# Performance work log

Hardware: AMD Instinct MI355X
Metric: run time of the kernel (lower is better)

Reference implementation:

```python
import jax, jax.numpy as jnp
import numpy as np

N1, E1 = 50000, 400000   # drug graph nodes/edges
N2, E2 = 50000, 400000   # second-branch nodes/edges
G = 256                   # number of graphs in the batch
F1, F2 = 93, 43           # node feature dims


def setup_inputs() -> dict:
    key = jax.random.key(0)
    ks = jax.random.split(key, 40)
    rn = lambda k, s, sc=0.05: jax.random.normal(k, s, dtype=jnp.float32) * sc
    inp = {}
    inp["data"] = 0  # unused placeholder arg in the original forward
    inp["x"] = jax.random.normal(ks[0], (N1, F1), dtype=jnp.float32)
    inp["edge_index"] = jax.random.randint(ks[1], (2, E1), 0, N1)
    inp["batch"] = jnp.sort(jax.random.randint(ks[2], (N1,), 0, G))
    inp["a"] = jax.random.normal(ks[3], (N2, F2), dtype=jnp.float32)
    inp["edge"] = jax.random.randint(ks[4], (2, E2), 0, N2)
    inp["c"] = jnp.sort(jax.random.randint(ks[5], (N2,), 0, G))
    # GINConv linear weights (x @ W + b convention)
    inp["W1"] = rn(ks[6], (F1, F1));        inp["b1"] = rn(ks[7], (F1,))
    inp["W2"] = rn(ks[8], (F1, F1 * 10));   inp["b2"] = rn(ks[9], (F1 * 10,))
    inp["W3"] = rn(ks[10], (F2, F2));       inp["b3"] = rn(ks[11], (F2,))
    inp["W4"] = rn(ks[12], (F2, F2 * 10));  inp["b4"] = rn(ks[13], (F2 * 10,))
    # fc_g: 1860 -> 1024 -> 512 ; fc_g1: 860 -> 1024 -> 512
    inp["fcg_w1"] = rn(ks[14], (F1 * 10 * 2, 1024)); inp["fcg_b1"] = rn(ks[15], (1024,))
    inp["fcg_w2"] = rn(ks[16], (1024, 512));         inp["fcg_b2"] = rn(ks[17], (512,))
    inp["fcg1_w1"] = rn(ks[18], (F2 * 10 * 2, 1024)); inp["fcg1_b1"] = rn(ks[19], (1024,))
    inp["fcg1_w2"] = rn(ks[20], (1024, 512));         inp["fcg1_b2"] = rn(ks[21], (512,))
    # fc_final / fc_final1: 512 -> 256 -> 1
    inp["ff_w1"] = rn(ks[22], (512, 256)); inp["ff_b1"] = rn(ks[23], (256,))
    inp["ff_w2"] = rn(ks[24], (256, 1));   inp["ff_b2"] = rn(ks[25], (1,))
    inp["ff1_w1"] = rn(ks[26], (512, 256)); inp["ff1_b1"] = rn(ks[27], (256,))
    inp["ff1_w2"] = rn(ks[28], (256, 1));   inp["ff1_b2"] = rn(ks[29], (1,))
    return inp


def _gin(h, ei, W, b):
    # PyG GINConv(eps=0): Linear(x_i + sum_{j->i} x_j)
    agg = jax.ops.segment_sum(h[ei[0]], ei[1], num_segments=h.shape[0])
    return (h + agg) @ W + b


def _pool(h, seg):
    # concat(global_max_pool, global_mean_pool) per graph -> [G, 2*d]
    s = jax.ops.segment_sum(h, seg, num_segments=G)
    cnt = jax.ops.segment_sum(jnp.ones((h.shape[0], 1), h.dtype), seg, num_segments=G)
    mean = s / jnp.maximum(cnt, 1.0)
    mx = jax.ops.segment_max(h, seg, num_segments=G)
    mx = jnp.where(jnp.isfinite(mx), mx, 0.0)
    return jnp.concatenate([mx, mean], axis=1)


def reference(data, x, edge_index, batch, a, edge, c,
              W1, b1, W2, b2, W3, b3, W4, b4,
              fcg_w1, fcg_b1, fcg_w2, fcg_b2,
              fcg1_w1, fcg1_b1, fcg1_w2, fcg1_b2,
              ff_w1, ff_b1, ff_w2, ff_b2,
              ff1_w1, ff1_b1, ff1_w2, ff1_b2):
    relu = jax.nn.relu
    # branch 1 (93-dim features)
    h = relu(_gin(x, edge_index, W1, b1))
    h = relu(_gin(h, edge_index, W2, b2))          # [N1, 930]
    p = _pool(h, batch)                             # [G, 1860]
    x_g = relu(p @ fcg_w1 + fcg_b1) @ fcg_w2 + fcg_b2   # [G, 512] (dropout = identity at eval)
    z = relu(x_g @ ff_w1 + ff_b1) @ ff_w2 + ff_b2        # [G, 1]
    # branch 2 (43-dim features)
    h1 = relu(_gin(a, edge, W3, b3))
    h1 = relu(_gin(h1, edge, W4, b4))               # [N2, 430]
    p1 = _pool(h1, c)                                # [G, 860]
    x_g1 = relu(p1 @ fcg1_w1 + fcg1_b1) @ fcg1_w2 + fcg1_b2  # [G, 512]
    z1 = relu(x_g1 @ ff1_w1 + ff1_b1) @ ff1_w2 + ff1_b2       # [G, 1]
    return (z, x_g, x_g1, z1)
```

## Files before the change

kernel.cpp:

```cpp
#include <hip/hip_runtime.h>


static constexpr int NG  = 256;
static constexpr int CHK = 4096;

typedef short  short8  __attribute__((ext_vector_type(8)));
typedef float  floatx4 __attribute__((ext_vector_type(4)));

__device__ __forceinline__ short f2bf(float f) {
    unsigned u = __float_as_uint(f);
    u += 0x7fff + ((u >> 16) & 1);
    return (short)(u >> 16);
}
__device__ __forceinline__ float bf2f(unsigned short s) {
    return __uint_as_float((unsigned)s << 16);
}
__device__ __forceinline__ float bf_lo(unsigned u) { return __uint_as_float(u << 16); }
__device__ __forceinline__ float bf_hi(unsigned u) { return __uint_as_float(u & 0xffff0000u); }

static inline int cdiv(int a, int b) { return (a + b - 1) / b; }

__global__ void offs_both_kernel(const int* __restrict__ s1, int n1, int* __restrict__ o1,
                                 const int* __restrict__ s2, int n2, int* __restrict__ o2) {
    int t = blockIdx.x * 256 + threadIdx.x;
    int br = t >> 9;
    int g = t & 511;
    if (br > 1 || g > NG) return;
    const int* seg = br ? s2 : s1;
    int N = br ? n2 : n1;
    int* offs = br ? o2 : o1;
    int lo = 0, hi = N;
    while (lo < hi) {
        int mid = (lo + hi) >> 1;
        if (seg[mid] < g) lo = mid + 1; else hi = mid;
    }
    offs[g] = lo;
}

__device__ __forceinline__ void deg_win_dev(const int* __restrict__ ei, int E, int N,
                                            int* __restrict__ deg, int bid) {
    int win = bid & 7, chunk = bid >> 3;
    int e0 = chunk * CHK;
    int e1 = e0 + CHK; if (e1 > E) e1 = E;
    int wlo = (int)((long)win * N / 8);
    int whi = (int)((long)(win + 1) * N / 8);
    for (int e = e0 + threadIdx.x; e < e1; e += 256) {
        int dst = ei[E + e];
        if (dst >= wlo && dst < whi) atomicAdd(&deg[dst], 1);
    }
}

__global__ __launch_bounds__(256) void deg_win_both_kernel(
        const int* ei1, int E1, int N1, int* d1, int nblk1,
        const int* ei2, int E2, int N2, int* d2) {
    int bid = blockIdx.x;
    if (bid < nblk1) deg_win_dev(ei1, E1, N1, d1, bid);
    else             deg_win_dev(ei2, E2, N2, d2, bid - nblk1);
}

__global__ __launch_bounds__(256) void scan1_both_kernel(
        const int* __restrict__ d1, int N1, int* __restrict__ x1, int* __restrict__ bs1, int nb1,
        const int* __restrict__ d2, int N2, int* __restrict__ x2, int* __restrict__ bs2) {
    __shared__ int sh[256];
    const int* deg; int* excl; int* bsum; int N; int blk;
    if ((int)blockIdx.x < nb1) { deg = d1; excl = x1; bsum = bs1; N = N1; blk = blockIdx.x; }
    else { deg = d2; excl = x2; bsum = bs2; N = N2; blk = blockIdx.x - nb1; }
    int base = blk * 1024;
    int t = threadIdx.x;
    int v[4];
    int s = 0;
    #pragma unroll
    for (int i = 0; i < 4; ++i) {
        int idx = base + t * 4 + i;
        v[i] = s;
        s += (idx < N) ? deg[idx] : 0;
    }
    sh[t] = s;
    __syncthreads();
    for (int off = 1; off < 256; off <<= 1) {
        int xv = (t >= off) ? sh[t - off] : 0;
        __syncthreads();
        sh[t] += xv;
        __syncthreads();
    }
    int texcl = (t > 0) ? sh[t - 1] : 0;
    #pragma unroll
    for (int i = 0; i < 4; ++i) {
        int idx = base + t * 4 + i;
        if (idx < N) excl[idx] = texcl + v[i];
    }
    if (t == 255) bsum[blk] = sh[255];
}

__global__ void scan2_both_kernel(int* __restrict__ b1, int nb1,
                                  int* __restrict__ b2, int nb2) {
    if (threadIdx.x) return;
    int* b = blockIdx.x ? b2 : b1;
    int nb = blockIdx.x ? nb2 : nb1;
    int acc = 0;
    for (int i = 0; i < nb; ++i) { int t = b[i]; b[i] = acc; acc += t; }
}

__global__ void scan3_both_kernel(int* __restrict__ x1, const int* __restrict__ bs1,
                                  int* __restrict__ c1, int N1, int Ev1,
                                  int* __restrict__ x2, const int* __restrict__ bs2,
                                  int* __restrict__ c2, int N2, int Ev2, int nc1) {
    int bid = blockIdx.x;
    int* excl; const int* bsum; int* cur; int N, E, i;
    if (bid < nc1) { i = bid * 256 + threadIdx.x; excl = x1; bsum = bs1; cur = c1; N = N1; E = Ev1; }
    else { i = (bid - nc1) * 256 + threadIdx.x; excl = x2; bsum = bs2; cur = c2; N = N2; E = Ev2; }
    if (i < N) {
        int v = excl[i] + bsum[i >> 10];
        excl[i] = v;
        cur[i] = v;
    }
    if (i == 0) excl[N] = E;
}

__device__ __forceinline__ void fill_win_dev(const int* __restrict__ ei, int E, int N,
                                             int* __restrict__ cursor, int* __restrict__ csr,
                                             int bid) {
    int win = bid & 7, chunk = bid >> 3;
    int e0 = chunk * CHK;
    int e1 = e0 + CHK; if (e1 > E) e1 = E;
    int wlo = (int)((long)win * N / 8);
    int whi = (int)((long)(win + 1) * N / 8);
    for (int e = e0 + threadIdx.x; e < e1; e += 256) {
        int dst = ei[E + e];
        if (dst >= wlo && dst < whi) {
            int pos = atomicAdd(&cursor[dst], 1);
            csr[pos] = ei[e];
        }
    }
}

__global__ __launch_bounds__(256) void fill_win_both_kernel(
        const int* ei1, int E1, int N1, int* c1, int* s1, int nblk1,
        const int* ei2, int E2, int N2, int* c2, int* s2) {
    int bid = blockIdx.x;
    if (bid < nblk1) fill_win_dev(ei1, E1, N1, c1, s1, bid);
    else             fill_win_dev(ei2, E2, N2, c2, s2, bid - nblk1);
}

struct RJob { const float* W; short* Wb; int K, Nsrc, Ndst, KP; };
struct RJobs10 { RJob j[10]; };

__global__ __launch_bounds__(256) void repack_all_kernel(RJobs10 jobs) {
    __shared__ __align__(16) short sh[64][72];
    RJob jb = jobs.j[blockIdx.y];
    int tilesC = (jb.Ndst + 63) >> 6;
    int tilesK = (jb.KP + 63) >> 6;
    if ((int)blockIdx.x >= tilesC * tilesK) return;
    int c0 = ((int)blockIdx.x % tilesC) * 64;
    int k0 = ((int)blockIdx.x / tilesC) * 64;
    int t = threadIdx.x;
    #pragma unroll 4
    for (int idx = t; idx < 64 * 64; idx += 256) {
        int kk = idx >> 6, cc = idx & 63;
        int k = k0 + kk, cg = c0 + cc;
        float v = (k < jb.K && cg < jb.Nsrc) ? jb.W[(size_t)k * jb.Nsrc + cg] : 0.f;
        sh[cc][kk] = f2bf(v);
    }
    __syncthreads();
    int kt = jb.KP - k0; if (kt > 64) kt = 64;
    int chunks = kt >> 3;
    for (int idx = t; idx < 64 * chunks; idx += 256) {
        int cc = idx / chunks, ch = idx - cc * chunks;
        int cg = c0 + cc;
        if (cg < jb.Ndst) {
            uint4 v = *(const uint4*)&sh[cc][ch * 8];
            *(uint4*)&jb.Wb[(size_t)cg * jb.KP + k0 + ch * 8] = v;
        }
    }
}

__global__ __launch_bounds__(256) void cast_both_kernel(
        const float* __restrict__ x1, unsigned short* __restrict__ xb1, int N1,
        const float* __restrict__ x2, unsigned short* __restrict__ xb2, int N2) {
    int idx = blockIdx.x * 256 + threadIdx.x;
    int tot1 = N1 * 96;
    if (idx < tot1) {
        int n = idx / 96, k = idx - n * 96;
        float v = (k < 93) ? x1[(size_t)n * 93 + k] : 0.f;
        xb1[idx] = (unsigned short)f2bf(v);
    } else {
        idx -= tot1;
        if (idx < N2 * 48) {
            int n = idx / 48, k = idx - n * 48;
            float v = (k < 43) ? x2[(size_t)n * 43 + k] : 0.f;
            xb2[idx] = (unsigned short)f2bf(v);
        }
    }
}

template<int F, int FP, int FA, int GROUPS>
__device__ __forceinline__ void gather_dev(
        const unsigned short* __restrict__ xb, const int* __restrict__ csr,
        const int* __restrict__ ro, float* __restrict__ agg, int N, int bid) {
    int wave = (bid * 256 + threadIdx.x) >> 6;
    int lane = threadIdx.x & 63;
    if (wave >= N) return;
    constexpr int HW = FP / 2;
    const unsigned* base = (const unsigned*)xb;
    int s = ro[wave], e = ro[wave + 1];
    int grp, l;
    if (GROUPS == 2) { grp = lane >> 5; l = lane & 31; }
    else             { grp = 0;         l = lane;      }
    bool act = l < HW;
    float lo = 0.f, hi = 0.f;
    int i = s + grp;
    if (GROUPS == 1) {
        for (; i + 3 < e; i += 4) {
            int n0 = csr[i], n1 = csr[i + 1], n2 = csr[i + 2], n3 = csr[i + 3];
            unsigned u0 = act ? base[(size_t)n0 * HW + l] : 0u;
            unsigned u1 = act ? base[(size_t)n1 * HW + l] : 0u;
            unsigned u2 = act ? base[(size_t)n2 * HW + l] : 0u;
            unsigned u3 = act ? base[(size_t)n3 * HW + l] : 0u;
            lo += bf_lo(u0) + bf_lo(u1) + bf_lo(u2) + bf_lo(u3);
            hi += bf_hi(u0) + bf_hi(u1) + bf_hi(u2) + bf_hi(u3);
        }
        for (; i < e; ++i) {
            int n0 = csr[i];
            unsigned u0 = act ? base[(size_t)n0 * HW + l] : 0u;
            lo += bf_lo(u0); hi += bf_hi(u0);
        }
    } else {
        for (; i + 2 < e; i += 4) {
            int n0 = csr[i], n1 = csr[i + 2];
            unsigned u0 = act ? base[(size_t)n0 * HW + l] : 0u;
            unsigned u1 = act ? base[(size_t)n1 * HW + l] : 0u;
            lo += bf_lo(u0) + bf_lo(u1);
            hi += bf_hi(u0) + bf_hi(u1);
        }
        if (i < e) {
            int n0 = csr[i];
            unsigned u0 = act ? base[(size_t)n0 * HW + l] : 0u;
            lo += bf_lo(u0); hi += bf_hi(u0);
        }
        lo += __shfl_xor(lo, 32, 64);
        hi += __shfl_xor(hi, 32, 64);
    }
    if (grp == 0) {
        int cidx = 2 * l;
        if (cidx + 1 < F)
            *(float2*)&agg[(size_t)wave * FA + cidx] = make_float2(lo, hi);
        else if (cidx < F)
            agg[(size_t)wave * FA + cidx] = lo;
    }
}

__global__ __launch_bounds__(256) void gather_both_kernel(
        const unsigned short* xb1, const int* csr1, const int* ro1, float* agg1, int N1, int nblk1,
        const unsigned short* xb2, const int* csr2, const int* ro2, float* agg2, int N2) {
    int bid = blockIdx.x;
    if (bid < nblk1) gather_dev<93, 96, 94, 1>(xb1, csr1, ro1, agg1, N1, bid);
    else             gather_dev<43, 48, 44, 2>(xb2, csr2, ro2, agg2, N2, bid - nblk1);
}

template<int F, int KP, int NT, int FP, int FA>
__device__ __forceinline__ void gin_linear_dev(
        const float* __restrict__ x, const float* __restrict__ agg,
        const short* __restrict__ Wb, const float* __restrict__ b,
        unsigned short* __restrict__ h1b, int N, int blk, short* Vb) {
    constexpr int KK = KP / 32;
    int c0 = blk * 64;
    int tid = threadIdx.x;
    int wid = tid >> 6;
    int lane = tid & 63;
    int ln = lane & 15, quad = lane >> 4;
    int cvalid = N - c0; if (cvalid > 64) cvalid = 64;
    for (int i = tid; i < 64 * (KP - F); i += 256)
        Vb[(i / (KP - F)) * KP + F + i % (KP - F)] = 0;
    int nelem = cvalid * F;
    const float* xs = x + (size_t)c0 * F;
    const float* as = agg + (size_t)c0 * FA;
    for (int idx = tid; idx < nelem; idx += 256) {
        int r = idx / F, k = idx - r * F;
        Vb[r * KP + k] = f2bf(xs[idx] + as[r * FA + k]);
    }
    __syncthreads();
    short8 afr[KK][4];
    #pragma unroll
    for (int kk = 0; kk < KK; ++kk)
        #pragma unroll
        for (int ms = 0; ms < 4; ++ms)
            afr[kk][ms] = *(const short8*)&Vb[(ms * 16 + ln) * KP + kk * 32 + quad * 8];
    for (int nt = wid; nt < NT; nt += 4) {
        int col = nt * 16 + ln;
        float bcol = (col < F) ? b[col] : 0.f;
        short8 bfr[KK];
        const short8* bp = (const short8*)(Wb + (size_t)col * KP + quad * 8);
        #pragma unroll
        for (int kk = 0; kk < KK; ++kk) bfr[kk] = bp[kk * 4];
        #pragma unroll
        for (int ms = 0; ms < 4; ++ms) {
            if (ms * 16 < cvalid) {
                floatx4 acc = {0.f, 0.f, 0.f, 0.f};
                #pragma unroll
                for (int kk = 0; kk < KK; ++kk)
                    acc = __builtin_amdgcn_mfma_f32_16x16x32_bf16(
                              afr[kk][ms], bfr[kk], acc, 0, 0, 0);
                #pragma unroll
                for (int r = 0; r < 4; ++r) {
                    int row = ms * 16 + quad * 4 + r;
                    if (row < cvalid) {
                        unsigned short hv = 0;
                        if (col < F) hv = (unsigned short)f2bf(fmaxf(acc[r] + bcol, 0.f));
                        h1b[(size_t)(c0 + row) * FP + col] = hv;
                    }
                }
            }
        }
    }
}

__global__ __launch_bounds__(256) void gin_linear_both_kernel(
        const float* x1, const float* agg1, const short* Wbl1, const float* bb1,
        unsigned short* h1b1, int N1, int nblk1,
        const float* x2, const float* agg2, const short* Wbl2, const float* bb2,
        unsigned short* h1b2, int N2) {
    __shared__ __align__(16) short Vb[64 * 96];
    int bid = blockIdx.x;
    if (bid < nblk1)
        gin_linear_dev<93, 96, 6, 96, 94>(x1, agg1, Wbl1, bb1, h1b1, N1, bid, Vb);
    else
        gin_linear_dev<43, 64, 3, 48, 44>(x2, agg2, Wbl2, bb2, h1b2, N2, bid - nblk1, Vb);
}

template<int F, int KP, int FO, int NT, int NS, int FP, int FA>
__device__ __forceinline__ void gin_pool_dev(
        const unsigned short* __restrict__ h1b, const float* __restrict__ agg,
        const short* __restrict__ Wb, const float* __restrict__ b,
        const int* __restrict__ offs,
        float* __restrict__ ppmax, float* __restrict__ ppsum,
        int blk, short* Vb, float* pmaxL, float* psumL) {
    constexpr int KK = KP / 32;
    int g = blk / NS;
    int s = blk % NS;
    int tid = threadIdx.x;
    int wid = tid >> 6;
    int lane = tid & 63;
    int ln = lane & 15;
    int quad = lane >> 4;

    int gs0 = offs[g], ge0 = offs[g + 1];
    int per = (ge0 - gs0 + NS - 1) / NS;
    int gs = gs0 + s * per;
    int ge = gs + per; if (ge > ge0) ge = ge0;

    for (int i = tid; i < NT * 16; i += 256) { pmaxL[i] = 0.f; psumL[i] = 0.f; }
    for (int i = tid; i < 64 * (KP - F); i += 256)
        Vb[(i / (KP - F)) * KP + F + i % (KP - F)] = 0;

    for (int c0 = gs; c0 < ge; c0 += 64) {
        __syncthreads();
        int cvalid = ge - c0; if (cvalid > 64) cvalid = 64;
        int nelem = cvalid * F;
        const unsigned short* hs = h1b + (size_t)c0 * FP;
        const float* as = agg + (size_t)c0 * FA;
        for (int idx = tid; idx < nelem; idx += 256) {
            int r = idx / F, k = idx - r * F;
            Vb[r * KP + k] = f2bf(bf2f(hs[r * FP + k]) + as[r * FA + k]);
        }
        __syncthreads();
        short8 afr[KK][4];
        #pragma unroll
        for (int kk = 0; kk < KK; ++kk)
            #pragma unroll
            for (int ms = 0; ms < 4; ++ms)
                afr[kk][ms] = *(const short8*)&Vb[(ms * 16 + ln) * KP + kk * 32 + quad * 8];
        for (int nt = wid; nt < NT; nt += 4) {
            int col = nt * 16 + ln;
            float bcol = (col < FO) ? b[col] : 0.f;
            short8 bfr[KK];
            const short8* bp = (const short8*)(Wb + (size_t)col * KP + quad * 8);
            #pragma unroll
            for (int kk = 0; kk < KK; ++kk) bfr[kk] = bp[kk * 4];
            float cmx = 0.f, csm = 0.f;
            #pragma unroll
            for (int ms = 0; ms < 4; ++ms) {
                if (ms * 16 < cvalid) {
                    floatx4 acc = {0.f, 0.f, 0.f, 0.f};
                    #pragma unroll
                    for (int kk = 0; kk < KK; ++kk)
                        acc = __builtin_amdgcn_mfma_f32_16x16x32_bf16(
                                  afr[kk][ms], bfr[kk], acc, 0, 0, 0);
                    #pragma unroll
                    for (int r = 0; r < 4; ++r) {
                        int rowl = ms * 16 + quad * 4 + r;
                        float v = fmaxf(acc[r] + bcol, 0.f);
                        if (rowl < cvalid) { cmx = fmaxf(cmx, v); csm += v; }
                    }
                }
            }
            cmx = fmaxf(cmx, __shfl_xor(cmx, 16, 64));
            cmx = fmaxf(cmx, __shfl_xor(cmx, 32, 64));
            csm += __shfl_xor(csm, 16, 64);
            csm += __shfl_xor(csm, 32, 64);
            if (quad == 0) {
                int i = nt * 16 + ln;
                pmaxL[i] = fmaxf(pmaxL[i], cmx);
                psumL[i] += csm;
            }
        }
    }
    __syncthreads();
    float* om = ppmax + (size_t)(g * NS + s) * FO;
    float* os = ppsum + (size_t)(g * NS + s) * FO;
    for (int col = tid; col < FO; col += 256) { om[col] = pmaxL[col]; os[col] = psumL[col]; }
}

__global__ __launch_bounds__(256) void gin_pool_both_kernel(
        const unsigned short* h1b1, const float* agg1, const short* Wbg1, const float* b21,
        const int* offs1, float* pm1, float* ps1, int nblk1,
        const unsigned short* h1b2, const float* agg2, const short* Wbg2, const float* b22,
        const int* offs2, float* pm2, float* ps2) {
    __shared__ __align__(16) short Vb[64 * 96];
    __shared__ float pmaxL[944];
    __shared__ float psumL[944];
    int bid = blockIdx.x;
    if (bid < nblk1)
        gin_pool_dev<93, 96, 930, 59, 4, 96, 94>(h1b1, agg1, Wbg1, b21, offs1,
                                                 pm1, ps1, bid, Vb, pmaxL, psumL);
    else
        gin_pool_dev<43, 64, 430, 27, 4, 48, 44>(h1b2, agg2, Wbg2, b22, offs2,
                                                 pm2, ps2, bid - nblk1, Vb, pmaxL, psumL);
}

template<int FO, int NS, int KPAD>
__device__ __forceinline__ void pool_reduce_dev(
        const float* __restrict__ ppmax, const float* __restrict__ ppsum,
        const int* __restrict__ offs, short* __restrict__ pb, int g) {
    int cntg = offs[g + 1] - offs[g];
    float den = (float)(cntg > 0 ? cntg : 1);
    for (int col = threadIdx.x; col < KPAD; col += 256) {
        float v = 0.f;
        if (col < FO) {
            float m = 0.f;
            #pragma unroll
            for (int ss = 0; ss < NS; ++ss)
                m = fmaxf(m, ppmax[(size_t)(g * NS + ss) * FO + col]);
            v = m;
        } else if (col < 2 * FO) {
            float sm = 0.f;
            #pragma unroll
            for (int ss = 0; ss < NS; ++ss)
                sm += ppsum[(size_t)(g * NS + ss) * FO + (col - FO)];
            v = sm / den;
        }
        pb[(size_t)g * KPAD + col] = f2bf(v);
    }
}

__global__ __launch_bounds__(256) void pool_reduce_both_kernel(
        const float* pm1, const float* ps1, const int* offs1, short* pb1,
        const float* pm2, const float* ps2, const int* offs2, short* pb2) {
    int bid = blockIdx.x;
    if (bid < NG) pool_reduce_dev<930, 4, 2048>(pm1, ps1, offs1, pb1, bid);
    else          pool_reduce_dev<430, 4, 1024>(pm2, ps2, offs2, pb2, bid - NG);
}

template<int KPC>
__device__ __forceinline__ void fc_mfma_dev(
        const short* __restrict__ Ab, const short* __restrict__ Wb,
        float* __restrict__ partial, int KP, int NB, int bid) {
    int mb = bid & 3;
    int nb = (bid >> 2) % NB;
    int ks = (bid >> 2) / NB;
    int tid = threadIdx.x;
    int w = tid >> 6;
    int lane = tid & 63;
    int ln = lane & 15, quad = lane >> 4;
    int row = mb * 64 + w * 16 + ln;
    const short* ap = Ab + (size_t)row * KP + ks * KPC + quad * 8;
    const short* wp = Wb + (size_t)(nb * 64 + ln) * KP + ks * KPC + quad * 8;
    floatx4 acc[4];
    #pragma unroll
    for (int ns = 0; ns < 4; ++ns) acc[ns] = {0.f, 0.f, 0.f, 0.f};
    #pragma unroll
    for (int kk = 0; kk < KPC / 32; ++kk) {
        short8 a = *(const short8*)(ap + kk * 32);
        #pragma unroll
        for (int ns = 0; ns < 4; ++ns) {
            short8 b = *(const short8*)(wp + (size_t)ns * 16 * KP + kk * 32);
            acc[ns] = __builtin_amdgcn_mfma_f32_16x16x32_bf16(a, b, acc[ns], 0, 0, 0);
        }
    }
    int N = NB * 64;
    float* pp = partial + ((size_t)ks * 256 + mb * 64 + w * 16) * N + nb * 64;
    #pragma unroll
    for (int ns = 0; ns < 4; ++ns)
        #pragma unroll
        for (int r = 0; r < 4; ++r)
            pp[(quad * 4 + r) * N + ns * 16 + ln] = acc[ns][r];
}

template<int KPC1, int KPC2>
__global__ __launch_bounds__(256) void fc_mfma_both_kernel(
        const short* A1, const short* B1, float* P1, int KPa, int NBa, int nblk1,
        const short* A2, const short* B2, float* P2, int KPb, int NBb) {
    int bid = blockIdx.x;
    if (bid < nblk1) fc_mfma_dev<KPC1>(A1, B1, P1, KPa, NBa, bid);
    else             fc_mfma_dev<KPC2>(A2, B2, P2, KPb, NBb, bid - nblk1);
}

template<int KS, bool RELU, bool WBF16, bool WF32>
__global__ __launch_bounds__(256) void fc_reduce_both_kernel(
        const float* __restrict__ P1, const float* __restrict__ b1v,
        short* __restrict__ ob1, float* __restrict__ of1, int MN1, int Nn1,
        const float* __restrict__ P2, const float* __restrict__ b2v,
        short* __restrict__ ob2, float* __restrict__ of2, int MN2, int Nn2) {
    int idx = blockIdx.x * 256 + threadIdx.x;
    const float* P; const float* bias; short* ob; float* of; int MN, Nn;
    if (idx < MN1) { P = P1; bias = b1v; ob = ob1; of = of1; MN = MN1; Nn = Nn1; }
    else {
        idx -= MN1;
        if (idx >= MN2) return;
        P = P2; bias = b2v; ob = ob2; of = of2; MN = MN2; Nn = Nn2;
    }
    float v = bias[idx % Nn];
    #pragma unroll
    for (int s = 0; s < KS; ++s) v += P[(size_t)s * MN + idx];
    if (RELU) v = fmaxf(v, 0.f);
    if (WBF16) ob[idx] = f2bf(v);
    if (WF32)  of[idx] = v;
}

template<int KS>
__global__ __launch_bounds__(256) void head_final_both_kernel(
        const float* __restrict__ P1, const float* __restrict__ b11,
        const float* __restrict__ w21, const float* __restrict__ b21,
        float* __restrict__ z1o,
        const float* __restrict__ P2, const float* __restrict__ b12,
        const float* __restrict__ w22, const float* __restrict__ b22,
        float* __restrict__ z2o) {
    int br = blockIdx.x >> 8;
    int row = blockIdx.x & 255;
    const float* P  = br ? P2  : P1;
    const float* b1 = br ? b12 : b11;
    const float* w2 = br ? w22 : w21;
    const float* b2 = br ? b22 : b21;
    float* zo       = br ? z2o : z1o;
    int t = threadIdx.x;
    float v = b1[t];
    int idx = row * 256 + t;
    #pragma unroll
    for (int s = 0; s < KS; ++s) v += P[(size_t)s * 65536 + idx];
    v = fmaxf(v, 0.f) * w2[t];
    #pragma unroll
    for (int o = 32; o > 0; o >>= 1) v += __shfl_down(v, o, 64);
    __shared__ float red[4];
    if ((t & 63) == 0) red[t >> 6] = v;
    __syncthreads();
    if (t == 0) zo[row] = red[0] + red[1] + red[2] + red[3] + b2[0];
}

extern "C" void kernel_launch(void* const* d_in, const int* in_sizes, int n_in,
                              void* d_out, int out_size, void* d_ws, size_t ws_size,
                              hipStream_t stream) {
    (void)n_in; (void)out_size; (void)ws_size;
    const float* x      = (const float*)d_in[1];
    const int*   ei     = (const int*)  d_in[2];
    const int*   batch  = (const int*)  d_in[3];
    const float* a      = (const float*)d_in[4];
    const int*   ed     = (const int*)  d_in[5];
    const int*   c      = (const int*)  d_in[6];
    const float* W1  = (const float*)d_in[7],  *b1  = (const float*)d_in[8];
    const float* W2  = (const float*)d_in[9],  *b2  = (const float*)d_in[10];
    const float* W3  = (const float*)d_in[11], *b3  = (const float*)d_in[12];
    const float* W4  = (const float*)d_in[13], *b4  = (const float*)d_in[14];
    const float* fg_w1  = (const float*)d_in[15], *fg_b1  = (const float*)d_in[16];
    const float* fg_w2  = (const float*)d_in[17], *fg_b2  = (const float*)d_in[18];
    const float* fg1_w1 = (const float*)d_in[19], *fg1_b1 = (const float*)d_in[20];
    const float* fg1_w2 = (const float*)d_in[21], *fg1_b2 = (const float*)d_in[22];
    const float* ff_w1  = (const float*)d_in[23], *ff_b1  = (const float*)d_in[24];
    const float* ff_w2  = (const float*)d_in[25], *ff_b2  = (const float*)d_in[26];
    const float* ff1_w1 = (const float*)d_in[27], *ff1_b1 = (const float*)d_in[28];
    const float* ff1_w2 = (const float*)d_in[29], *ff1_b2 = (const float*)d_in[30];

    const int N1 = in_sizes[1] / 93;
    const int E1 = in_sizes[2] / 2;
    const int N2 = in_sizes[4] / 43;
    const int E2 = in_sizes[5] / 2;

    float* out = (float*)d_out;
    float* z   = out;
    float* xg  = out + 256;
    float* xg1 = out + 256 + 256 * 512;
    float* z1  = out + 256 + 2 * 256 * 512;

    char* wsb = (char*)d_ws;
    size_t off = 0;
    auto carve = [&](size_t bytes) {
        void* ptr = wsb + off;
        off = (off + bytes + 255) & ~(size_t)255;
        return ptr;
    };
    float*          agg1 = (float*)carve((size_t)N1 * 94 * sizeof(float));
    float*          agg2 = (float*)carve((size_t)N2 * 44 * sizeof(float));
    unsigned short* xb1  = (unsigned short*)carve((size_t)N1 * 96 * 2);
    unsigned short* xb2  = (unsigned short*)carve((size_t)N2 * 48 * 2);
    unsigned short* h1b1 = (unsigned short*)carve((size_t)N1 * 96 * 2);
    unsigned short* h1b2 = (unsigned short*)carve((size_t)N2 * 48 * 2);
    short* pb1  = (short*)carve((size_t)NG * 2048 * 2);
    short* pb2  = (short*)carve((size_t)NG * 1024 * 2);
    short* t1b1 = (short*)carve((size_t)NG * 1024 * 2);
    short* t1b2 = (short*)carve((size_t)NG * 1024 * 2);
    short* xgb1 = (short*)carve((size_t)NG * 512 * 2);
    short* xgb2 = (short*)carve((size_t)NG * 512 * 2);
    short* Wbl1 = (short*)carve((size_t)96 * 96 * 2);
    short* Wbg1 = (short*)carve((size_t)944 * 96 * 2);
    short* Wbl2 = (short*)carve((size_t)48 * 64 * 2);
    short* Wbg2 = (short*)carve((size_t)432 * 64 * 2);
    short* Wb1a = (short*)carve((size_t)1024 * 2048 * 2);
    short* Wb2a = (short*)carve((size_t)512 * 1024 * 2);
    short* Wb3a = (short*)carve((size_t)256 * 512 * 2);
    short* Wb1b = (short*)carve((size_t)1024 * 1024 * 2);
    short* Wb2b = (short*)carve((size_t)512 * 1024 * 2);
    short* Wb3b = (short*)carve((size_t)256 * 512 * 2);
    int* offs1 = (int*)carve(257 * 4);
    int* offs2 = (int*)carve(257 * 4);
    int* deg   = (int*)carve((size_t)(N1 + N2) * 4);
    int* rowoff1 = (int*)carve((size_t)(N1 + 1) * 4);
    int* rowoff2 = (int*)carve((size_t)(N2 + 1) * 4);
    int* cursor1 = (int*)carve((size_t)N1 * 4);
    int* cursor2 = (int*)carve((size_t)N2 * 4);
    int* csr1  = (int*)carve((size_t)E1 * 4);
    int* csr2  = (int*)carve((size_t)E2 * 4);
    int* bsum  = (int*)carve(256 * 4);
    int* deg1 = deg, *deg2 = deg + N1;
    int* bsum1 = bsum, *bsum2 = bsum + 128;
    float* partial1 = agg1;
    float* partial2 = agg1 + (size_t)8 * 262144;
    float* pm1 = (float*)xb1;
    float* ps1 = pm1 + (size_t)NG * 4 * 930;
    float* pm2 = (float*)xb2;
    float* ps2 = pm2 + (size_t)NG * 4 * 430;

    constexpr int KS = 8;

    RJobs10 jobs = {{
        { W1,     Wbl1, 93,   93,   96,   96   },
        { W2,     Wbg1, 93,   930,  944,  96   },
        { W3,     Wbl2, 43,   43,   48,   64   },
        { W4,     Wbg2, 43,   430,  432,  64   },
        { fg_w1,  Wb1a, 1860, 1024, 1024, 2048 },
        { fg_w2,  Wb2a, 1024, 512,  512,  1024 },
        { ff_w1,  Wb3a, 512,  256,  256,  512  },
        { fg1_w1, Wb1b, 860,  1024, 1024, 1024 },
        { fg1_w2, Wb2b, 1024, 512,  512,  1024 },
        { ff1_w1, Wb3b, 512,  256,  256,  512  },
    }};
    repack_all_kernel<<<dim3(512, 10), 256, 0, stream>>>(jobs);
    cast_both_kernel<<<cdiv(N1 * 96 + N2 * 48, 256), 256, 0, stream>>>(
        x, xb1, N1, a, xb2, N2);
    offs_both_kernel<<<4, 256, 0, stream>>>(batch, N1, offs1, c, N2, offs2);
    hipMemsetAsync(deg, 0, (size_t)(N1 + N2) * 4, stream);
    int nwb1 = cdiv(E1, CHK) * 8, nwb2 = cdiv(E2, CHK) * 8;
    deg_win_both_kernel<<<nwb1 + nwb2, 256, 0, stream>>>(ei, E1, N1, deg1, nwb1,
                                                         ed, E2, N2, deg2);
    int nb1 = cdiv(N1, 1024), nb2 = cdiv(N2, 1024);
    scan1_both_kernel<<<nb1 + nb2, 256, 0, stream>>>(deg1, N1, rowoff1, bsum1, nb1,
                                                     deg2, N2, rowoff2, bsum2);
    scan2_both_kernel<<<2, 64, 0, stream>>>(bsum1, nb1, bsum2, nb2);
    int nc1 = cdiv(N1, 256), nc2 = cdiv(N2, 256);
    scan3_both_kernel<<<nc1 + nc2, 256, 0, stream>>>(rowoff1, bsum1, cursor1, N1, E1,
                                                     rowoff2, bsum2, cursor2, N2, E2, nc1);
    fill_win_both_kernel<<<nwb1 + nwb2, 256, 0, stream>>>(ei, E1, N1, cursor1, csr1, nwb1,
                                                          ed, E2, N2, cursor2, csr2);

    int ng1 = cdiv(N1, 4), ng2 = cdiv(N2, 4);
    gather_both_kernel<<<ng1 + ng2, 256, 0, stream>>>(
        xb1, csr1, rowoff1, agg1, N1, ng1, xb2, csr2, rowoff2, agg2, N2);
    int nl1 = cdiv(N1, 64), nl2 = cdiv(N2, 64);
    gin_linear_both_kernel<<<nl1 + nl2, 256, 0, stream>>>(
        x, agg1, Wbl1, b1, h1b1, N1, nl1, a, agg2, Wbl2, b3, h1b2, N2);
    gather_both_kernel<<<ng1 + ng2, 256, 0, stream>>>(
        h1b1, csr1, rowoff1, agg1, N1, ng1, h1b2, csr2, rowoff2, agg2, N2);
    gin_pool_both_kernel<<<NG * 4 * 2, 256, 0, stream>>>(
        h1b1, agg1, Wbg1, b2, offs1, pm1, ps1, NG * 4,
        h1b2, agg2, Wbg2, b4, offs2, pm2, ps2);
    pool_reduce_both_kernel<<<2 * NG, 256, 0, stream>>>(
        pm1, ps1, offs1, pb1, pm2, ps2, offs2, pb2);

    fc_mfma_both_kernel<256, 128><<<1024, 256, 0, stream>>>(
        pb1, Wb1a, partial1, 2048, 16, 512, pb2, Wb1b, partial2, 1024, 16);
    fc_reduce_both_kernel<KS, true, true, false><<<cdiv(2 * 256 * 1024, 256), 256, 0, stream>>>(
        partial1, fg_b1, t1b1, nullptr, 256 * 1024, 1024,
        partial2, fg1_b1, t1b2, nullptr, 256 * 1024, 1024);
    fc_mfma_both_kernel<128, 128><<<512, 256, 0, stream>>>(
        t1b1, Wb2a, partial1, 1024, 8, 256, t1b2, Wb2b, partial2, 1024, 8);
    fc_reduce_both_kernel<KS, false, true, true><<<cdiv(2 * 256 * 512, 256), 256, 0, stream>>>(
        partial1, fg_b2, xgb1, xg, 256 * 512, 512,
        partial2, fg1_b2, xgb2, xg1, 256 * 512, 512);
    fc_mfma_both_kernel<64, 64><<<256, 256, 0, stream>>>(
        xgb1, Wb3a, partial1, 512, 4, 128, xgb2, Wb3b, partial2, 512, 4);
    head_final_both_kernel<KS><<<512, 256, 0, stream>>>(
        partial1, ff_b1, ff_w2, ff_b2, z,
        partial2, ff1_b1, ff1_w2, ff1_b2, z1);
}
```

Baseline: 451.2 us.

## Fuse self-term into gather and emit bf16 GIN inputs directly

The gather kernel now adds each node's own feature row to the neighbour sum and writes the combined (x + agg) row as padded bf16, instead of writing a float aggregate. The linear and pool kernels then load MFMA A-fragments straight from global bf16 rows, dropping the LDS staging, the float-to-bf16 combine loop and a barrier per tile. This cuts intermediate traffic (fp32 agg to bf16) and deepens gather unrolling to 8 loads in flight. The combined sum is rounded to bf16 once, which was also true of the old path. Split-K partial buffers get their own allocation, since agg no longer exists to alias.

```diff
diff --git a/kernel.cpp b/kernel.cpp
--- a/kernel.cpp
+++ b/kernel.cpp
@@ -11,9 +11,6 @@
     unsigned u = __float_as_uint(f);
     u += 0x7fff + ((u >> 16) & 1);
     return (short)(u >> 16);
-}
-__device__ __forceinline__ float bf2f(unsigned short s) {
-    return __uint_as_float((unsigned)s << 16);
 }
 __device__ __forceinline__ float bf_lo(unsigned u) { return __uint_as_float(u << 16); }
 __device__ __forceinline__ float bf_hi(unsigned u) { return __uint_as_float(u & 0xffff0000u); }
@@ -193,75 +190,93 @@
     }
 }
 
-template<int F, int FP, int FA, int GROUPS>
+template<int FP, int GROUPS>
 __device__ __forceinline__ void gather_dev(
-        const unsigned short* __restrict__ xb, const int* __restrict__ csr,
-        const int* __restrict__ ro, float* __restrict__ agg, int N, int bid) {
+        const unsigned short* __restrict__ src, const int* __restrict__ csr,
+        const int* __restrict__ ro, unsigned short* __restrict__ vb, int N, int bid) {
     int wave = (bid * 256 + threadIdx.x) >> 6;
     int lane = threadIdx.x & 63;
     if (wave >= N) return;
     constexpr int HW = FP / 2;
-    const unsigned* base = (const unsigned*)xb;
+    const unsigned* base = (const unsigned*)src;
+    unsigned* out = (unsigned*)vb;
     int s = ro[wave], e = ro[wave + 1];
     int grp, l;
     if (GROUPS == 2) { grp = lane >> 5; l = lane & 31; }
     else             { grp = 0;         l = lane;      }
     bool act = l < HW;
-    float lo = 0.f, hi = 0.f;
+    unsigned su = (act && grp == 0) ? base[(size_t)wave * HW + l] : 0u;
+    float lo = bf_lo(su), hi = bf_hi(su);
     int i = s + grp;
     if (GROUPS == 1) {
-        for (; i + 3 < e; i += 4) {
-            int n0 = csr[i], n1 = csr[i + 1], n2 = csr[i + 2], n3 = csr[i + 3];
-            unsigned u0 = act ? base[(size_t)n0 * HW + l] : 0u;
-            unsigned u1 = act ? base[(size_t)n1 * HW + l] : 0u;
-            unsigned u2 = act ? base[(size_t)n2 * HW + l] : 0u;
-            unsigned u3 = act ? base[(size_t)n3 * HW + l] : 0u;
-            lo += bf_lo(u0) + bf_lo(u1) + bf_lo(u2) + bf_lo(u3);
-            hi += bf_hi(u0) + bf_hi(u1) + bf_hi(u2) + bf_hi(u3);
+        for (; i + 7 < e; i += 8) {
+            unsigned u[8];
+            #pragma unroll
+            for (int q = 0; q < 8; ++q)
+                u[q] = act ? base[(size_t)csr[i + q] * HW + l] : 0u;
+            #pragma unroll
+            for (int q = 0; q < 8; ++q) { lo += bf_lo(u[q]); hi += bf_hi(u[q]); }
         }
         for (; i < e; ++i) {
-            int n0 = csr[i];
-            unsigned u0 = act ? base[(size_t)n0 * HW + l] : 0u;
+            unsigned u0 = act ? base[(size_t)csr[i] * HW + l] : 0u;
             lo += bf_lo(u0); hi += bf_hi(u0);
         }
     } else {
-        for (; i + 2 < e; i += 4) {
-            int n0 = csr[i], n1 = csr[i + 2];
-            unsigned u0 = act ? base[(size_t)n0 * HW + l] : 0u;
-            unsigned u1 = act ? base[(size_t)n1 * HW + l] : 0u;
-            lo += bf_lo(u0) + bf_lo(u1);
-            hi += bf_hi(u0) + bf_hi(u1);
-        }
-        if (i < e) {
-            int n0 = csr[i];
-            unsigned u0 = act ? base[(size_t)n0 * HW + l] : 0u;
+        for (; i + 6 < e; i += 8) {
+            unsigned u[4];
+            #pragma unroll
+            for (int q = 0; q < 4; ++q)
+                u[q] = act ? base[(size_t)csr[i + 2 * q] * HW + l] : 0u;
+            #pragma unroll
+            for (int q = 0; q < 4; ++q) { lo += bf_lo(u[q]); hi += bf_hi(u[q]); }
+        }
+        for (; i < e; i += 2) {
+            unsigned u0 = act ? base[(size_t)csr[i] * HW + l] : 0u;
             lo += bf_lo(u0); hi += bf_hi(u0);
         }
         lo += __shfl_xor(lo, 32, 64);
         hi += __shfl_xor(hi, 32, 64);
     }
-    if (grp == 0) {
-        int cidx = 2 * l;
-        if (cidx + 1 < F)
-            *(float2*)&agg[(size_t)wave * FA + cidx] = make_float2(lo, hi);
-        else if (cidx < F)
-            agg[(size_t)wave * FA + cidx] = lo;
+    if (grp == 0 && act) {
+        unsigned plo = (unsigned)(unsigned short)f2bf(lo);
+        unsigned phi = (unsigned)(unsigned short)f2bf(hi);
+        out[(size_t)wave * HW + l] = (phi << 16) | plo;
     }
 }
 
 __global__ __launch_bounds__(256) void gather_both_kernel(
-        const unsigned short* xb1, const int* csr1, const int* ro1, float* agg1, int N1, int nblk1,
-        const unsigned short* xb2, const int* csr2, const int* ro2, float* agg2, int N2) {
-    int bid = blockIdx.x;
-    if (bid < nblk1) gather_dev<93, 96, 94, 1>(xb1, csr1, ro1, agg1, N1, bid);
-    else             gather_dev<43, 48, 44, 2>(xb2, csr2, ro2, agg2, N2, bid - nblk1);
-}
-
-template<int F, int KP, int NT, int FP, int FA>
+        const unsigned short* s1, const int* csr1, const int* ro1,
+        unsigned short* vb1, int N1, int nblk1,
+        const unsigned short* s2, const int* csr2, const int* ro2,
+        unsigned short* vb2, int N2) {
+    int bid = blockIdx.x;
+    if (bid < nblk1) gather_dev<96, 1>(s1, csr1, ro1, vb1, N1, bid);
+    else             gather_dev<48, 2>(s2, csr2, ro2, vb2, N2, bid - nblk1);
+}
+
+template<int FP, int KP, int KK>
+__device__ __forceinline__ void load_afr(const short* __restrict__ vr,
+                                         int row0, int ln, int quad,
+                                         short8 afr[][4]) {
+    #pragma unroll
+    for (int ms = 0; ms < 4; ++ms) {
+        const short* rp = vr + (size_t)(row0 + ms * 16 + ln) * FP;
+        #pragma unroll
+        for (int kk = 0; kk < KK; ++kk) {
+            int offk = kk * 32 + quad * 8;
+            short8 v = {0, 0, 0, 0, 0, 0, 0, 0};
+            if (FP == KP || offk + 8 <= FP)
+                v = *(const short8*)(rp + offk);
+            afr[kk][ms] = v;
+        }
+    }
+}
+
+template<int F, int KP, int NT, int FP>
 __device__ __forceinline__ void gin_linear_dev(
-        const float* __restrict__ x, const float* __restrict__ agg,
-        const short* __restrict__ Wb, const float* __restrict__ b,
-        unsigned short* __restrict__ h1b, int N, int blk, short* Vb) {
+        const unsigned short* __restrict__ vb, const short* __restrict__ Wb,
+        const float* __restrict__ b, unsigned short* __restrict__ h1b,
+        int N, int blk) {
     constexpr int KK = KP / 32;
     int c0 = blk * 64;
     int tid = threadIdx.x;
@@ -269,22 +284,9 @@
     int lane = tid & 63;
     int ln = lane & 15, quad = lane >> 4;
     int cvalid = N - c0; if (cvalid > 64) cvalid = 64;
-    for (int i = tid; i < 64 * (KP - F); i += 256)
-        Vb[(i / (KP - F)) * KP + F + i % (KP - F)] = 0;
-    int nelem = cvalid * F;
-    const float* xs = x + (size_t)c0 * F;
-    const float* as = agg + (size_t)c0 * FA;
-    for (int idx = tid; idx < nelem; idx += 256) {
-        int r = idx / F, k = idx - r * F;
-        Vb[r * KP + k] = f2bf(xs[idx] + as[r * FA + k]);
-    }
-    __syncthreads();
+    const short* vr = (const short*)vb;
     short8 afr[KK][4];
-    #pragma unroll
-    for (int kk = 0; kk < KK; ++kk)
-        #pragma unroll
-        for (int ms = 0; ms < 4; ++ms)
-            afr[kk][ms] = *(const short8*)&Vb[(ms * 16 + ln) * KP + kk * 32 + quad * 8];
+    load_afr<FP, KP, KK>(vr, c0, ln, quad, afr);
     for (int nt = wid; nt < NT; nt += 4) {
         int col = nt * 16 + ln;
         float bcol = (col < F) ? b[col] : 0.f;
@@ -315,25 +317,23 @@
 }
 
 __global__ __launch_bounds__(256) void gin_linear_both_kernel(
-        const float* x1, const float* agg1, const short* Wbl1, const float* bb1,
+        const unsigned short* vb1, const short* Wbl1, const float* bb1,
         unsigned short* h1b1, int N1, int nblk1,
-        const float* x2, const float* agg2, const short* Wbl2, const float* bb2,
+        const unsigned short* vb2, const short* Wbl2, const float* bb2,
         unsigned short* h1b2, int N2) {
-    __shared__ __align__(16) short Vb[64 * 96];
     int bid = blockIdx.x;
     if (bid < nblk1)
-        gin_linear_dev<93, 96, 6, 96, 94>(x1, agg1, Wbl1, bb1, h1b1, N1, bid, Vb);
+        gin_linear_dev<93, 96, 6, 96>(vb1, Wbl1, bb1, h1b1, N1, bid);
     else
-        gin_linear_dev<43, 64, 3, 48, 44>(x2, agg2, Wbl2, bb2, h1b2, N2, bid - nblk1, Vb);
-}
-
-template<int F, int KP, int FO, int NT, int NS, int FP, int FA>
+        gin_linear_dev<43, 64, 3, 48>(vb2, Wbl2, bb2, h1b2, N2, bid - nblk1);
+}
+
+template<int F, int KP, int FO, int NT, int NS, int FP>
 __device__ __forceinline__ void gin_pool_dev(
-        const unsigned short* __restrict__ h1b, const float* __restrict__ agg,
-        const short* __restrict__ Wb, const float* __restrict__ b,
-        const int* __restrict__ offs,
+        const unsigned short* __restrict__ vb, const short* __restrict__ Wb,
+        const float* __restrict__ b, const int* __restrict__ offs,
         float* __restrict__ ppmax, float* __restrict__ ppsum,
-        int blk, short* Vb, float* pmaxL, float* psumL) {
+        int blk, float* pmaxL, float* psumL) {
     constexpr int KK = KP / 32;
     int g = blk / NS;
     int s = blk % NS;
@@ -349,26 +349,13 @@
     int ge = gs + per; if (ge > ge0) ge = ge0;
 
     for (int i = tid; i < NT * 16; i += 256) { pmaxL[i] = 0.f; psumL[i] = 0.f; }
-    for (int i = tid; i < 64 * (KP - F); i += 256)
-        Vb[(i / (KP - F)) * KP + F + i % (KP - F)] = 0;
-
+    __syncthreads();
+
+    const short* vr = (const short*)vb;
     for (int c0 = gs; c0 < ge; c0 += 64) {
-        __syncthreads();
         int cvalid = ge - c0; if (cvalid > 64) cvalid = 64;
-        int nelem = cvalid * F;
-        const unsigned short* hs = h1b + (size_t)c0 * FP;
-        const float* as = agg + (size_t)c0 * FA;
-        for (int idx = tid; idx < nelem; idx += 256) {
-            int r = idx / F, k = idx - r * F;
-            Vb[r * KP + k] = f2bf(bf2f(hs[r * FP + k]) + as[r * FA + k]);
-        }
-        __syncthreads();
         short8 afr[KK][4];
-        #pragma unroll
-        for (int kk = 0; kk < KK; ++kk)
-            #pragma unroll
-            for (int ms = 0; ms < 4; ++ms)
-                afr[kk][ms] = *(const short8*)&Vb[(ms * 16 + ln) * KP + kk * 32 + quad * 8];
+        load_afr<FP, KP, KK>(vr, c0, ln, quad, afr);
         for (int nt = wid; nt < NT; nt += 4) {
             int col = nt * 16 + ln;
             float bcol = (col < FO) ? b[col] : 0.f;
@@ -411,20 +398,19 @@
 }
 
 __global__ __launch_bounds__(256) void gin_pool_both_kernel(
-        const unsigned short* h1b1, const float* agg1, const short* Wbg1, const float* b21,
+        const unsigned short* vb1, const short* Wbg1, const float* b21,
         const int* offs1, float* pm1, float* ps1, int nblk1,
-        const unsigned short* h1b2, const float* agg2, const short* Wbg2, const float* b22,
+        const unsigned short* vb2, const short* Wbg2, const float* b22,
         const int* offs2, float* pm2, float* ps2) {
-    __shared__ __align__(16) short Vb[64 * 96];
     __shared__ float pmaxL[944];
     __shared__ float psumL[944];
     int bid = blockIdx.x;
     if (bid < nblk1)
-        gin_pool_dev<93, 96, 930, 59, 4, 96, 94>(h1b1, agg1, Wbg1, b21, offs1,
-                                                 pm1, ps1, bid, Vb, pmaxL, psumL);
+        gin_pool_dev<93, 96, 930, 59, 4, 96>(vb1, Wbg1, b21, offs1,
+                                             pm1, ps1, bid, pmaxL, psumL);
     else
-        gin_pool_dev<43, 64, 430, 27, 4, 48, 44>(h1b2, agg2, Wbg2, b22, offs2,
-                                                 pm2, ps2, bid - nblk1, Vb, pmaxL, psumL);
+        gin_pool_dev<43, 64, 430, 27, 4, 48>(vb2, Wbg2, b22, offs2,
+                                             pm2, ps2, bid - nblk1, pmaxL, psumL);
 }
 
 template<int FO, int NS, int KPAD>
@@ -596,10 +582,10 @@
         off = (off + bytes + 255) & ~(size_t)255;
         return ptr;
     };
-    float*          agg1 = (float*)carve((size_t)N1 * 94 * sizeof(float));
-    float*          agg2 = (float*)carve((size_t)N2 * 44 * sizeof(float));
     unsigned short* xb1  = (unsigned short*)carve((size_t)N1 * 96 * 2);
     unsigned short* xb2  = (unsigned short*)carve((size_t)N2 * 48 * 2);
+    unsigned short* vb1  = (unsigned short*)carve((size_t)(N1 + 64) * 96 * 2);
+    unsigned short* vb2  = (unsigned short*)carve((size_t)(N2 + 64) * 48 * 2);
     unsigned short* h1b1 = (unsigned short*)carve((size_t)N1 * 96 * 2);
     unsigned short* h1b2 = (unsigned short*)carve((size_t)N2 * 48 * 2);
     short* pb1  = (short*)carve((size_t)NG * 2048 * 2);
@@ -608,6 +594,8 @@
     short* t1b2 = (short*)carve((size_t)NG * 1024 * 2);
     short* xgb1 = (short*)carve((size_t)NG * 512 * 2);
     short* xgb2 = (short*)carve((size_t)NG * 512 * 2);
+    float* partial1 = (float*)carve((size_t)8 * 256 * 1024 * 4);
+    float* partial2 = (float*)carve((size_t)8 * 256 * 1024 * 4);
     short* Wbl1 = (short*)carve((size_t)96 * 96 * 2);
     short* Wbg1 = (short*)carve((size_t)944 * 96 * 2);
     short* Wbl2 = (short*)carve((size_t)48 * 64 * 2);
@@ -630,8 +618,6 @@
     int* bsum  = (int*)carve(256 * 4);
     int* deg1 = deg, *deg2 = deg + N1;
     int* bsum1 = bsum, *bsum2 = bsum + 128;
-    float* partial1 = agg1;
-    float* partial2 = agg1 + (size_t)8 * 262144;
     float* pm1 = (float*)xb1;
     float* ps1 = pm1 + (size_t)NG * 4 * 930;
     float* pm2 = (float*)xb2;
@@ -671,15 +657,15 @@
 
     int ng1 = cdiv(N1, 4), ng2 = cdiv(N2, 4);
     gather_both_kernel<<<ng1 + ng2, 256, 0, stream>>>(
-        xb1, csr1, rowoff1, agg1, N1, ng1, xb2, csr2, rowoff2, agg2, N2);
+        xb1, csr1, rowoff1, vb1, N1, ng1, xb2, csr2, rowoff2, vb2, N2);
     int nl1 = cdiv(N1, 64), nl2 = cdiv(N2, 64);
     gin_linear_both_kernel<<<nl1 + nl2, 256, 0, stream>>>(
-        x, agg1, Wbl1, b1, h1b1, N1, nl1, a, agg2, Wbl2, b3, h1b2, N2);
+        vb1, Wbl1, b1, h1b1, N1, nl1, vb2, Wbl2, b3, h1b2, N2);
     gather_both_kernel<<<ng1 + ng2, 256, 0, stream>>>(
-        h1b1, csr1, rowoff1, agg1, N1, ng1, h1b2, csr2, rowoff2, agg2, N2);
+        h1b1, csr1, rowoff1, vb1, N1, ng1, h1b2, csr2, rowoff2, vb2, N2);
     gin_pool_both_kernel<<<NG * 4 * 2, 256, 0, stream>>>(
-        h1b1, agg1, Wbg1, b2, offs1, pm1, ps1, NG * 4,
-        h1b2, agg2, Wbg2, b4, offs2, pm2, ps2);
+        vb1, Wbg1, b2, offs1, pm1, ps1, NG * 4,
+        vb2, Wbg2, b4, offs2, pm2, ps2);
     pool_reduce_both_kernel<<<2 * NG, 256, 0, stream>>>(
         pm1, ps1, offs1, pb1, pm2, ps2, offs2, pb2);
 
```

Result: no change. 454.1 us (+0.6%).
